# Kernel tuning notes

Hardware: AMD Instinct MI355X
Metric: run time of the kernel (lower is better)

The kernel has to match this reference:

```python
import jax, jax.numpy as jnp
import numpy as np

B, T, DIM, S, DFF = 4, 2048, 2048, 4, 8192
SINKHORN_ITERS = 10


def setup_inputs() -> dict:
    key = jax.random.key(0)
    ks = jax.random.split(key, 12)

    def lin(k, fan_in, shape):
        bound = 1.0 / np.sqrt(fan_in)
        return jax.random.uniform(k, shape, jnp.float32, -bound, bound)

    return {
        "x": jax.random.normal(ks[0], (B, T, DIM), jnp.float32),
        # phi_* linears act on the S-times tiled vector of size S*DIM
        "phi_pre_w": lin(ks[1], S * DIM, (S, S * DIM)),
        "phi_pre_b": lin(ks[2], S * DIM, (S,)),
        "phi_post_w": lin(ks[3], S * DIM, (S, S * DIM)),
        "phi_post_b": lin(ks[4], S * DIM, (S,)),
        "phi_res_w": lin(ks[5], S * DIM, (S * S, S * DIM)),
        "phi_res_b": lin(ks[6], S * DIM, (S * S,)),
        "alpha_pre": jnp.ones((1,), jnp.float32),
        "alpha_post": jnp.ones((1,), jnp.float32),
        "alpha_res": jnp.ones((1,), jnp.float32),
        "b_pre": jnp.zeros((S,), jnp.float32),
        "b_post": jnp.zeros((S,), jnp.float32),
        "b_res": jnp.zeros((S, S), jnp.float32),
        # block = transformer MLP
        "W1": lin(ks[7], DIM, (DIM, DFF)),
        "b1": lin(ks[8], DIM, (DFF,)),
        "W2": lin(ks[9], DFF, (DFF, DIM)),
        "b2": lin(ks[10], DFF, (DIM,)),
    }


def sinkhorn_knopp(logits):
    # logits: [B, T, S, S] -> doubly-stochastic via exp + alternating normalization
    M = jnp.exp(logits)
    for _ in range(SINKHORN_ITERS):
        M = M / jnp.sum(M, axis=-1, keepdims=True)  # rows
        M = M / jnp.sum(M, axis=-2, keepdims=True)  # cols
    return M


def reference(x, phi_pre_w, phi_pre_b, phi_post_w, phi_post_b, phi_res_w,
              phi_res_b, alpha_pre, alpha_post, alpha_res, b_pre, b_post,
              b_res, W1, b1, W2, b2):
    bs, seq, d = x.shape
    s = b_pre.shape[0]
    eps = jnp.asarray(jnp.finfo(x.dtype).eps, x.dtype)
    # x_l = x expanded over S identical streams; x_vec = tile(x, S).
    # RMS over the tiled S*d vector == RMS over d (streams are copies).
    x_n = x * jax.lax.rsqrt(jnp.mean(x * x, axis=-1, keepdims=True) + eps)
    # Linear on the tiled vector == sum of the S weight blocks applied to x_n.
    Wp = phi_pre_w.reshape(s, s, d).sum(axis=1)        # [S, d]
    Wq = phi_post_w.reshape(s, s, d).sum(axis=1)       # [S, d]
    Wr = phi_res_w.reshape(s * s, s, d).sum(axis=1)    # [S*S, d]
    h_pre_t = alpha_pre * (jnp.einsum('btd,sd->bts', x_n, Wp) + phi_pre_b) + b_pre
    h_post_t = alpha_post * (jnp.einsum('btd,sd->bts', x_n, Wq) + phi_post_b) + b_post
    h_res_t = alpha_res * (jnp.einsum('btd,kd->btk', x_n, Wr) + phi_res_b)
    h_res_t = h_res_t.reshape(bs, seq, s, s) + b_res
    h_pre = jax.nn.sigmoid(h_pre_t)                    # [B,T,S]
    h_post = 2.0 * jax.nn.sigmoid(h_post_t)            # [B,T,S]
    h_res = sinkhorn_knopp(h_res_t)                    # [B,T,S,S]
    # block_input = sum_j x_l[:,:,j] * h_pre[...,j] ; streams identical -> x * sum_j h_pre
    block_input = x * jnp.sum(h_pre, axis=-1, keepdims=True)
    # block: MLP with exact (erf) GELU, matching torch default
    h = jax.nn.gelu(jnp.einsum('btd,df->btf', block_input, W1) + b1, approximate=False)
    block_out = jnp.einsum('btf,fd->btd', h, W2) + b2
    # out = sum_i [ (h_res @ x_l)_i + h_post_i * block_out ]
    #     = x * sum_{ij} h_res[ij] + block_out * sum_i h_post_i
    res_mix = jnp.sum(h_res, axis=(-2, -1))[..., None]         # [B,T,1]
    post_mix = jnp.sum(h_post, axis=-1, keepdims=True)          # [B,T,1]
    return x * res_mix + block_out * post_mix
```

## Files before the change

kernel.cpp:

```cpp
#include <hip/hip_runtime.h>
#include <hip/hip_bf16.h>
#include <cstdint>
#include <cstddef>

#define DIM   2048
#define DFF   8192
#define NROWS 8192
#define NFOLD 24

typedef float f32x4 __attribute__((ext_vector_type(4)));
typedef __bf16 bf16x8 __attribute__((ext_vector_type(8)));

__device__ __forceinline__ float sigmoidf_(float v) { return 1.0f / (1.0f + expf(-v)); }

__device__ __forceinline__ unsigned short f2bf(float v) {
    union { __hip_bfloat16 h; unsigned short u; } cv;
    cv.h = __float2bfloat16(v);
    return cv.u;
}

__device__ __forceinline__ void async_copy16(const void* g, void* l) {
    __builtin_amdgcn_global_load_lds((const __attribute__((address_space(1))) void*)g,
                                     (__attribute__((address_space(3))) void*)l, 16, 0, 0);
}

__device__ __forceinline__ void wg_barrier() {
    asm volatile("" ::: "memory");
    __builtin_amdgcn_s_barrier();
    asm volatile("" ::: "memory");
}

#define VM(n)  asm volatile("s_waitcnt vmcnt(" #n ")" ::: "memory")
#define LGKM0  asm volatile("s_waitcnt lgkmcnt(0)" ::: "memory")
#define LGKM8  asm volatile("s_waitcnt lgkmcnt(8)" ::: "memory")

__global__ __launch_bounds__(256) void fold_kernel(const float* __restrict__ pre_w,
                                                   const float* __restrict__ post_w,
                                                   const float* __restrict__ res_w,
                                                   float* __restrict__ Wfold) {
    int idx = blockIdx.x * 256 + threadIdx.x;
    if (idx >= NFOLD * DIM) return;
    int r = idx >> 11;
    int d = idx & (DIM - 1);
    const float* src;
    if (r < 4)      src = pre_w  + (size_t)r * (4 * DIM);
    else if (r < 8) src = post_w + (size_t)(r - 4) * (4 * DIM);
    else            src = res_w  + (size_t)(r - 8) * (4 * DIM);
    Wfold[idx] = src[d] + src[DIM + d] + src[2 * DIM + d] + src[3 * DIM + d];
}

__global__ __launch_bounds__(256) void transpose_to_bf16(const float* __restrict__ in,
                                                         __hip_bfloat16* __restrict__ out,
                                                         int R, int C) {
    __shared__ float tile[32][33];
    int bx = blockIdx.x, by = blockIdx.y;
    int tx = threadIdx.x & 31, ty0 = threadIdx.x >> 5;
#pragma unroll
    for (int i = 0; i < 4; i++) {
        int ty = ty0 + i * 8;
        tile[ty][tx] = in[(size_t)(by * 32 + ty) * C + bx * 32 + tx];
    }
    __syncthreads();
#pragma unroll
    for (int i = 0; i < 4; i++) {
        int ty = ty0 + i * 8;
        out[(size_t)(bx * 32 + ty) * R + by * 32 + tx] = __float2bfloat16(tile[tx][ty]);
    }
}

__global__ __launch_bounds__(512) void gating_kernel(
    const float* __restrict__ x, const float* __restrict__ Wfold,
    const float* __restrict__ phi_pre_b, const float* __restrict__ phi_post_b,
    const float* __restrict__ phi_res_b,
    const float* __restrict__ alpha_pre, const float* __restrict__ alpha_post,
    const float* __restrict__ alpha_res,
    const float* __restrict__ b_pre, const float* __restrict__ b_post,
    const float* __restrict__ b_res,
    __hip_bfloat16* __restrict__ Abuf,
    float* __restrict__ g_res_arr, float* __restrict__ g_post_arr) {
    const int tid = threadIdx.x;
    const int lane = tid & 63, wave = tid >> 6;
    const int row = blockIdx.x * 8 + wave;

    const float4* x4 = (const float4*)x + (size_t)row * 512;
    const float4* w4 = (const float4*)Wfold;

    float4 xv[8];
#pragma unroll
    for (int j = 0; j < 8; j++) xv[j] = x4[j * 64 + lane];

    float p[25];
    p[24] = 0.f;
#pragma unroll
    for (int j = 0; j < 8; j++)
        p[24] += xv[j].x * xv[j].x + xv[j].y * xv[j].y + xv[j].z * xv[j].z + xv[j].w * xv[j].w;

    for (int r = 0; r < NFOLD; r++) {
        float acc = 0.f;
#pragma unroll
        for (int j = 0; j < 8; j++) {
            float4 wv = w4[r * 512 + j * 64 + lane];
            acc += xv[j].x * wv.x + xv[j].y * wv.y + xv[j].z * wv.z + xv[j].w * wv.w;
        }
        p[r] = acc;
    }

#pragma unroll
    for (int r = 0; r < 25; r++) {
        float v = p[r];
#pragma unroll
        for (int off = 1; off < 64; off <<= 1) v += __shfl_xor(v, off, 64);
        p[r] = v;
    }

    const float rms = rsqrtf(p[24] / (float)DIM + 1.1920928955078125e-07f);
    const float ap = alpha_pre[0], aq = alpha_post[0], ar = alpha_res[0];
    float gpre = 0.f, gpost = 0.f;
#pragma unroll
    for (int s = 0; s < 4; s++) {
        gpre  += sigmoidf_(ap * (rms * p[s]     + phi_pre_b[s])  + b_pre[s]);
        gpost += 2.0f * sigmoidf_(aq * (rms * p[4 + s] + phi_post_b[s]) + b_post[s]);
    }
    float Mm[4][4];
#pragma unroll
    for (int i = 0; i < 4; i++)
#pragma unroll
        for (int j = 0; j < 4; j++) {
            int k = i * 4 + j;
            Mm[i][j] = expf(ar * (rms * p[8 + k] + phi_res_b[k]) + b_res[k]);
        }
    for (int it = 0; it < 10; ++it) {
#pragma unroll
        for (int i = 0; i < 4; i++) {
            float rs = 1.0f / (Mm[i][0] + Mm[i][1] + Mm[i][2] + Mm[i][3]);
#pragma unroll
            for (int j = 0; j < 4; j++) Mm[i][j] *= rs;
        }
#pragma unroll
        for (int j = 0; j < 4; j++) {
            float cs = 1.0f / (Mm[0][j] + Mm[1][j] + Mm[2][j] + Mm[3][j]);
#pragma unroll
            for (int i = 0; i < 4; i++) Mm[i][j] *= cs;
        }
    }
    float gres = 0.f;
#pragma unroll
    for (int i = 0; i < 4; i++)
#pragma unroll
        for (int j = 0; j < 4; j++) gres += Mm[i][j];

    __hip_bfloat16* arow = Abuf + (size_t)row * DIM;
#pragma unroll
    for (int j = 0; j < 8; j++) {
        ushort4 u;
        u.x = f2bf(xv[j].x * gpre); u.y = f2bf(xv[j].y * gpre);
        u.z = f2bf(xv[j].z * gpre); u.w = f2bf(xv[j].w * gpre);
        *reinterpret_cast<ushort4*>(arow + (j * 64 + lane) * 4) = u;
    }
    if (lane == 0) {
        g_res_arr[row]  = gres;
        g_post_arr[row] = gpost;
    }
}

#define RD_A(DST, REG)                                                            \
    _Pragma("unroll") for (int m = 0; m < 4; ++m) {                               \
        DST[m][0] = *(const bf16x8*)((REG) + baseA + m * 2048 + cb0);             \
        DST[m][1] = *(const bf16x8*)((REG) + baseA + m * 2048 + cb1);             \
    }
#define RD_B(DST, REG)                                                            \
    _Pragma("unroll") for (int n = 0; n < 2; ++n) {                               \
        DST[n][0] = *(const bf16x8*)((REG) + baseB + n * 2048 + cb0);             \
        DST[n][1] = *(const bf16x8*)((REG) + baseB + n * 2048 + cb1);             \
    }

#define MQ(AF, BF, MO, NO)                                                        \
    __builtin_amdgcn_s_setprio(1);                                                \
    _Pragma("unroll") for (int m = 0; m < 4; ++m)                                 \
    _Pragma("unroll") for (int n = 0; n < 2; ++n) {                               \
        acc[(MO) + m][(NO) + n] = __builtin_amdgcn_mfma_f32_16x16x32_bf16(        \
            AF[m][0], BF[n][0], acc[(MO) + m][(NO) + n], 0, 0, 0);                \
        acc[(MO) + m][(NO) + n] = __builtin_amdgcn_mfma_f32_16x16x32_bf16(        \
            AF[m][1], BF[n][1], acc[(MO) + m][(NO) + n], 0, 0, 0);                \
    }                                                                             \
    __builtin_amdgcn_s_setprio(0);

#define STG_A(t_, h_)                                                             \
    if ((t_) < nk) {                                                              \
        char* l_ = ldsA + (((t_) & 1) * 32768) + (h_) * 16384 + wave * 1024;      \
        async_copy16(Ab + aOff[0][h_] + (size_t)(t_) * 128, l_);                  \
        async_copy16(Ab + aOff[1][h_] + (size_t)(t_) * 128, l_ + 8192);           \
    }
#define STG_B(t_, h_)                                                             \
    if ((t_) < nk) {                                                              \
        char* l_ = ldsB + (((t_) & 1) * 32768) + (h_) * 16384 + wave * 1024;      \
        async_copy16(Bb + bOff[0][h_] + (size_t)(t_) * 128, l_);                  \
        async_copy16(Bb + bOff[1][h_] + (size_t)(t_) * 128, l_ + 8192);           \
    }

template <int MODE, int NB>
__global__ __launch_bounds__(512, 2) void gemm256(
    const __hip_bfloat16* __restrict__ A, const __hip_bfloat16* __restrict__ Bt,
    int M, int N, int K, const float* __restrict__ bias,
    __hip_bfloat16* __restrict__ outh, float* __restrict__ outf,
    const float* __restrict__ x, const float* __restrict__ g_res,
    const float* __restrict__ g_post) {
    __shared__ __align__(16) char ldsA[65536];
    __shared__ __align__(16) char ldsB[65536];

    const int wg = blockIdx.x;
    const int xcd = wg & 7;
    const int i = wg >> 3;
    const int nt = xcd * NB + (i % NB);
    const int mt = i / NB;
    const int m0 = mt * 256;
    const int n0 = nt * 256;

    const int tid = threadIdx.x;
    const int lane = tid & 63;
    const int wave = tid >> 6;
    const int wr = wave >> 2;
    const int wc = wave & 3;
    const int q = lane >> 4;
    const int rr = lane & 7;

    const uint32_t cb0 = (uint32_t)((q ^ rr) << 4);
    const uint32_t cb1 = (uint32_t)(((4 + q) ^ rr) << 4);
    const uint32_t baseA = (uint32_t)((wr * 64 + (lane & 15)) * 128);
    const uint32_t baseB = (uint32_t)((wc * 32 + (lane & 15)) * 128);

    const uint32_t scb = (uint32_t)((((lane & 7) ^ ((lane >> 3) & 7))) << 4);
    const int lr = lane >> 3;
    const size_t K2 = (size_t)K * 2;
    size_t aOff[2][2], bOff[2][2];
#pragma unroll
    for (int ii = 0; ii < 2; ++ii)
#pragma unroll
        for (int h = 0; h < 2; ++h) {
            int gA = m0 + wave * 8 + lr + ii * 128 + h * 64;
            int gB = n0 + ((wave >> 2) + 2 * ii) * 64 + h * 32 + (wave & 3) * 8 + lr;
            aOff[ii][h] = (size_t)gA * K2 + scb;
            bOff[ii][h] = (size_t)gB * K2 + scb;
        }
    const char* Ab = (const char*)A;
    const char* Bb = (const char*)Bt;

    f32x4 acc[8][4];
#pragma unroll
    for (int m = 0; m < 8; ++m)
#pragma unroll
        for (int n = 0; n < 4; ++n) acc[m][n] = (f32x4){0.f, 0.f, 0.f, 0.f};

    const int nk = K / 64;

    STG_A(0, 0); STG_B(0, 0); STG_B(0, 1); STG_A(0, 1);
    STG_A(1, 0); STG_B(1, 0); STG_A(1, 1);
    VM(6);
    wg_barrier();

    bf16x8 a0[4][2], a1[4][2];
    bf16x8 b0[2][2], b1[2][2];

    for (int kt = 0; kt < nk; ++kt) {
        const int c = kt & 1;
        const char* Ac = ldsA + c * 32768;
        const char* Bc = ldsB + c * 32768;
        RD_A(a0, Ac)
        RD_B(b0, Bc)
        STG_B(kt + 1, 1)
        LGKM8;
        wg_barrier();
        LGKM0;
        MQ(a0, b0, 0, 0)
        wg_barrier();
        RD_B(b1, Bc + 16384)
        STG_A(kt + 2, 0)
        wg_barrier();
        LGKM0;
        MQ(a0, b1, 0, 2)
        wg_barrier();
        RD_A(a1, Ac + 16384)
        STG_B(kt + 2, 0)
        wg_barrier();
        LGKM0;
        MQ(a1, b0, 4, 0)
        wg_barrier();
        STG_A(kt + 2, 1)
        if (kt + 2 < nk) { VM(6); } else { VM(0); }
        wg_barrier();
        MQ(a1, b1, 4, 2)
        wg_barrier();
    }

#pragma unroll
    for (int mi = 0; mi < 8; ++mi) {
#pragma unroll
        for (int ni = 0; ni < 4; ++ni) {
            const int col = n0 + wc * 64 + (ni >> 1) * 32 + (ni & 1) * 16 + (lane & 15);
            const float bc = bias[col];
#pragma unroll
            for (int j = 0; j < 4; ++j) {
                const int row = m0 + wr * 128 + (mi >> 2) * 64 + (mi & 3) * 16 + q * 4 + j;
                float v = acc[mi][ni][j] + bc;
                if (MODE == 1) {
                    float u = 1.5957691216057308f * (v + 0.044715f * v * v * v);
                    float s = 1.0f / (1.0f + __expf(-u));
                    outh[(size_t)row * N + col] = __float2bfloat16(v * s);
                } else {
                    outf[(size_t)row * N + col] =
                        x[(size_t)row * N + col] * g_res[row] + v * g_post[row];
                }
            }
        }
    }
}

extern "C" void kernel_launch(void* const* d_in, const int* in_sizes, int n_in,
                              void* d_out, int out_size, void* d_ws, size_t ws_size,
                              hipStream_t stream) {
    const float* x          = (const float*)d_in[0];
    const float* phi_pre_w  = (const float*)d_in[1];
    const float* phi_pre_b  = (const float*)d_in[2];
    const float* phi_post_w = (const float*)d_in[3];
    const float* phi_post_b = (const float*)d_in[4];
    const float* phi_res_w  = (const float*)d_in[5];
    const float* phi_res_b  = (const float*)d_in[6];
    const float* alpha_pre  = (const float*)d_in[7];
    const float* alpha_post = (const float*)d_in[8];
    const float* alpha_res  = (const float*)d_in[9];
    const float* b_pre      = (const float*)d_in[10];
    const float* b_post     = (const float*)d_in[11];
    const float* b_res      = (const float*)d_in[12];
    const float* W1         = (const float*)d_in[13];
    const float* b1         = (const float*)d_in[14];
    const float* W2         = (const float*)d_in[15];
    const float* b2         = (const float*)d_in[16];
    float* out = (float*)d_out;

    char* ws = (char*)d_ws;
    __hip_bfloat16* W1T  = (__hip_bfloat16*)ws;
    __hip_bfloat16* W2T  = W1T + (size_t)DFF * DIM;
    __hip_bfloat16* Abuf = W2T + (size_t)DIM * DFF;
    __hip_bfloat16* Hbuf = Abuf + (size_t)NROWS * DIM;
    float* Wfold = (float*)(Hbuf + (size_t)NROWS * DFF);
    float* gres  = Wfold + NFOLD * DIM;
    float* gpost = gres + NROWS;

    fold_kernel<<<(NFOLD * DIM + 255) / 256, 256, 0, stream>>>(phi_pre_w, phi_post_w,
                                                               phi_res_w, Wfold);
    transpose_to_bf16<<<dim3(DFF / 32, DIM / 32), 256, 0, stream>>>(W1, W1T, DIM, DFF);
    transpose_to_bf16<<<dim3(DIM / 32, DFF / 32), 256, 0, stream>>>(W2, W2T, DFF, DIM);
    gating_kernel<<<NROWS / 8, 512, 0, stream>>>(x, Wfold, phi_pre_b, phi_post_b, phi_res_b,
                                                 alpha_pre, alpha_post, alpha_res,
                                                 b_pre, b_post, b_res, Abuf, gres, gpost);
    gemm256<1, 4><<<1024, 512, 0, stream>>>(
        Abuf, W1T, NROWS, DFF, DIM, b1, Hbuf, nullptr, nullptr, nullptr, nullptr);
    gemm256<2, 1><<<256, 512, 0, stream>>>(
        Hbuf, W2T, NROWS, DIM, DFF, b2, nullptr, out, x, gres, gpost);
}
```

Measured before the change: 651.4 us.

## Ping-pong wave groups so one half computes MFMA while other loads LDS

Splits the eight waves of the GEMM workgroup into two groups by row. The groups alternate between issuing LDS reads and global-to-LDS stages and running MFMA quadrants, with barriers between phases, so matrix math from one group overlaps memory work from the other. The second group prefetches the next tile's fragments at the end of each iteration. This adds more barriers per k-step and more complex ordering of the shared-buffer hazards, which could introduce stalls or races if the stage/wait counts are off.

```diff
diff --git a/kernel.cpp b/kernel.cpp
--- a/kernel.cpp
+++ b/kernel.cpp
@@ -32,7 +32,6 @@
 
 #define VM(n)  asm volatile("s_waitcnt vmcnt(" #n ")" ::: "memory")
 #define LGKM0  asm volatile("s_waitcnt lgkmcnt(0)" ::: "memory")
-#define LGKM8  asm volatile("s_waitcnt lgkmcnt(8)" ::: "memory")
 
 __global__ __launch_bounds__(256) void fold_kernel(const float* __restrict__ pre_w,
                                                    const float* __restrict__ post_w,
@@ -223,6 +222,7 @@
     const int wc = wave & 3;
     const int q = lane >> 4;
     const int rr = lane & 7;
+    const bool gA = (wr == 0);
 
     const uint32_t cb0 = (uint32_t)((q ^ rr) << 4);
     const uint32_t cb1 = (uint32_t)(((4 + q) ^ rr) << 4);
@@ -237,10 +237,10 @@
     for (int ii = 0; ii < 2; ++ii)
 #pragma unroll
         for (int h = 0; h < 2; ++h) {
-            int gA = m0 + wave * 8 + lr + ii * 128 + h * 64;
-            int gB = n0 + ((wave >> 2) + 2 * ii) * 64 + h * 32 + (wave & 3) * 8 + lr;
-            aOff[ii][h] = (size_t)gA * K2 + scb;
-            bOff[ii][h] = (size_t)gB * K2 + scb;
+            int gAr = m0 + wave * 8 + lr + ii * 128 + h * 64;
+            int gBr = n0 + ((wave >> 2) + 2 * ii) * 64 + h * 32 + (wave & 3) * 8 + lr;
+            aOff[ii][h] = (size_t)gAr * K2 + scb;
+            bOff[ii][h] = (size_t)gBr * K2 + scb;
         }
     const char* Ab = (const char*)A;
     const char* Bb = (const char*)Bt;
@@ -260,35 +260,50 @@
 
     bf16x8 a0[4][2], a1[4][2];
     bf16x8 b0[2][2], b1[2][2];
+    if (!gA) {
+        RD_A(a0, ldsA)
+        RD_B(b0, ldsB)
+        LGKM0;
+    }
+    wg_barrier();
 
     for (int kt = 0; kt < nk; ++kt) {
-        const int c = kt & 1;
-        const char* Ac = ldsA + c * 32768;
-        const char* Bc = ldsB + c * 32768;
-        RD_A(a0, Ac)
-        RD_B(b0, Bc)
-        STG_B(kt + 1, 1)
-        LGKM8;
-        wg_barrier();
-        LGKM0;
-        MQ(a0, b0, 0, 0)
-        wg_barrier();
-        RD_B(b1, Bc + 16384)
-        STG_A(kt + 2, 0)
-        wg_barrier();
-        LGKM0;
-        MQ(a0, b1, 0, 2)
-        wg_barrier();
-        RD_A(a1, Ac + 16384)
-        STG_B(kt + 2, 0)
-        wg_barrier();
-        LGKM0;
-        MQ(a1, b0, 4, 0)
-        wg_barrier();
-        STG_A(kt + 2, 1)
-        if (kt + 2 < nk) { VM(6); } else { VM(0); }
-        wg_barrier();
-        MQ(a1, b1, 4, 2)
+        const char* Ac = ldsA + (kt & 1) * 32768;
+        const char* Bc = ldsB + (kt & 1) * 32768;
+        const char* An = ldsA + ((kt + 1) & 1) * 32768;
+        const char* Bn = ldsB + ((kt + 1) & 1) * 32768;
+        if (gA) { RD_A(a0, Ac) RD_B(b0, Bc) STG_B(kt + 1, 1) LGKM0; }
+        else    { MQ(a0, b0, 0, 0) }
+        wg_barrier();
+        if (gA) { MQ(a0, b0, 0, 0) }
+        else    { RD_B(b1, Bc + 16384) STG_B(kt + 1, 1) LGKM0; }
+        wg_barrier();
+        if (gA) { RD_B(b1, Bc + 16384) STG_A(kt + 2, 0) LGKM0; }
+        else    { MQ(a0, b1, 0, 2) }
+        wg_barrier();
+        if (gA) { MQ(a0, b1, 0, 2) }
+        else    { RD_A(a1, Ac + 16384) STG_A(kt + 2, 0) LGKM0; }
+        wg_barrier();
+        if (gA) { RD_A(a1, Ac + 16384) STG_B(kt + 2, 0) LGKM0; }
+        else    { MQ(a1, b0, 4, 0) }
+        wg_barrier();
+        if (gA) { MQ(a1, b0, 4, 0) }
+        else    { STG_B(kt + 2, 0) }
+        wg_barrier();
+        if (gA) {
+            STG_A(kt + 2, 1)
+            if (kt + 2 < nk) { VM(6); } else { VM(0); }
+        } else {
+            MQ(a1, b1, 4, 2)
+        }
+        wg_barrier();
+        if (gA) {
+            MQ(a1, b1, 4, 2)
+        } else {
+            STG_A(kt + 2, 1)
+            if (kt + 2 < nk) { VM(6); } else { VM(0); }
+            if (kt + 1 < nk) { RD_A(a0, An) RD_B(b0, Bn) LGKM0; }
+        }
         wg_barrier();
     }
 
```

Result: slower. 748.0 us (+14.8%).
